# Kernel tuning notes

Measured on AMD Instinct MI355X. Metric: run time of the kernel, lower is better.

The kernel has to match this reference:

```python
import jax, jax.numpy as jnp
import numpy as np

NUM_SAMPLED = 8192
NUM_CLASSES = 50000
DIM = 512
BATCH = 8192


def _log_uniform_expected(ids, num_sampled, num_classes):
    # log-uniform sampler probability: P(c) = (log(c+2) - log(c+1)) / log(V+1)
    c = ids.astype(jnp.float32)
    p = (jnp.log(c + 2.0) - jnp.log(c + 1.0)) / jnp.log(float(num_classes + 1))
    # expected count under unique sampling of num_sampled candidates (as in TF)
    return -jnp.expm1(float(num_sampled) * jnp.log1p(-p))


def setup_inputs() -> dict:
    key = jax.random.key(0)
    k1, k2, k3, k4, k5 = jax.random.split(key, 5)
    inputs = jax.random.normal(k1, (BATCH, DIM), jnp.float32)
    labels = jax.random.randint(k2, (BATCH, 1), 0, NUM_CLASSES)
    kernel = jax.random.uniform(k3, (NUM_CLASSES, DIM), jnp.float32, -0.05, 0.05)
    bias = jax.random.uniform(k4, (NUM_CLASSES,), jnp.float32, -0.05, 0.05)
    sampled = jax.random.randint(k5, (NUM_SAMPLED,), 0, NUM_CLASSES)
    return {"inputs": inputs, "labels": labels, "kernel": kernel,
            "bias": bias, "sampled": sampled}


def reference(inputs, labels, kernel, bias, sampled):
    # tf.nn.sampled_softmax_loss (train branch), num_true=1,
    # log-uniform sampler, remove_accidental_hits=True.
    labels_flat = labels[:, 0]

    # true logits: gather one weight row per example, dot with input
    w_true = kernel[labels_flat]                      # [B, D]
    b_true = bias[labels_flat]                        # [B]
    true_logits = jnp.einsum('bd,bd->b', inputs, w_true) + b_true
    true_logits = true_logits - jnp.log(
        _log_uniform_expected(labels_flat, NUM_SAMPLED, NUM_CLASSES))

    # sampled logits: gather S candidate rows, small matmul [B,D]x[D,S]
    w_samp = kernel[sampled]                          # [S, D]
    b_samp = bias[sampled]                            # [S]
    sampled_logits = jnp.einsum('bd,sd->bs', inputs, w_samp) + b_samp[None, :]
    sampled_logits = sampled_logits - jnp.log(
        _log_uniform_expected(sampled, NUM_SAMPLED, NUM_CLASSES))

    # remove accidental hits: mask sampled candidates that equal the true label
    hits = labels_flat[:, None] == sampled[None, :]   # [B, S]
    sampled_logits = jnp.where(hits, -1e9, sampled_logits)

    # softmax CE with the true class at column 0
    logits = jnp.concatenate([true_logits[:, None], sampled_logits], axis=1)
    loss = jax.nn.logsumexp(logits, axis=1) - logits[:, 0]  # [B]
    return loss
```

## Files before the change

### kernel.cpp

```cpp
#include <hip/hip_runtime.h>
#include <hip/hip_bf16.h>
#include <cstdint>
#include <cstddef>

#define BATCH   8192
#define NSAMP   8192
#define DIM     512
#define NCLASS  50000

typedef __attribute__((ext_vector_type(8))) short bf16x8;
typedef __attribute__((ext_vector_type(4))) float f32x4;

__device__ __forceinline__ float neg_log_expected(int c) {
    double p = log1p(1.0 / (double)(c + 1)) / log((double)(NCLASS + 1));
    double e = -expm1((double)NSAMP * log1p(-p));
    return (float)(-log(e));
}

__device__ __forceinline__ unsigned short f2bf(float f) {
    __hip_bfloat16 h = __float2bfloat16(f);
    return *reinterpret_cast<unsigned short*>(&h);
}

__device__ __forceinline__ void gload_lds16(const void* g, void* l) {
    __builtin_amdgcn_global_load_lds(
        (const __attribute__((address_space(1))) void*)g,
        (__attribute__((address_space(3))) void*)l, 16, 0, 0);
}

__global__ void k_fused(const float* __restrict__ inputs, const int* __restrict__ labels,
                        const float* __restrict__ W, const float* __restrict__ bias,
                        __hip_bfloat16* __restrict__ Abf,
                        float* __restrict__ true_logit, float* __restrict__ row_sum) {
    int row = blockIdx.x;
    int t   = threadIdx.x;
    float4 v = reinterpret_cast<const float4*>(inputs + (size_t)row * DIM)[t];
    ushort4 u;
    u.x = f2bf(v.x); u.y = f2bf(v.y); u.z = f2bf(v.z); u.w = f2bf(v.w);
    reinterpret_cast<ushort4*>(Abf + (size_t)row * DIM)[t] = u;

    int lbl = labels[row];
    float4 w = reinterpret_cast<const float4*>(W + (size_t)lbl * DIM)[t];
    float dot = v.x * w.x + v.y * w.y + v.z * w.z + v.w * w.w;
    #pragma unroll
    for (int off = 32; off; off >>= 1) dot += __shfl_down(dot, off, 64);
    __shared__ float red[2];
    if ((t & 63) == 0) red[t >> 6] = dot;
    __syncthreads();
    if (t == 0) {
        float tl = red[0] + red[1] + bias[lbl] + neg_log_expected(lbl);
        true_logit[row] = tl;
        row_sum[row]    = __expf(tl);
    }
}

__global__ void k_gather(const float* __restrict__ W, const float* __restrict__ bias,
                         const int* __restrict__ sampled,
                         __hip_bfloat16* __restrict__ Bbf, float* __restrict__ adj) {
    int s   = blockIdx.x;
    int idx = sampled[s];
    float4 v = reinterpret_cast<const float4*>(W + (size_t)idx * DIM)[threadIdx.x];
    ushort4 u;
    u.x = f2bf(v.x); u.y = f2bf(v.y); u.z = f2bf(v.z); u.w = f2bf(v.w);
    reinterpret_cast<ushort4*>(Bbf + (size_t)s * DIM)[threadIdx.x] = u;
    if (threadIdx.x == 0) adj[s] = bias[idx] + neg_log_expected(idx);
}

__global__ __launch_bounds__(256, 4) void k_gemm(
    const __hip_bfloat16* __restrict__ A, const __hip_bfloat16* __restrict__ B,
    const float* __restrict__ adj, const int* __restrict__ labels,
    const int* __restrict__ sampled, float* __restrict__ row_sum) {
    __shared__ alignas(16) __hip_bfloat16 Asm[2][128 * 32];
    __shared__ alignas(16) __hip_bfloat16 Bsm[2][128 * 32];
    __shared__ float tsum[2][128];

    const int tid  = threadIdx.x;
    const int wave = tid >> 6;
    const int lane = tid & 63;
    const int wr   = wave >> 1;
    const int wc   = wave & 1;

    const int bid  = blockIdx.x;
    const int xcd  = bid & 7;
    const int u    = bid >> 3;
    const int rb   = xcd * 8 + (u & 7);
    const int cgrp = u >> 3;
    const int brow = rb * 128;

    const int srow = lane >> 2;
    const int sg   = (lane & 3) ^ ((lane >> 3) & 3);
    const int rsel = lane & 15;
    const int koff = ((lane >> 4) ^ ((lane >> 1) & 3)) * 8;

    f32x4 acc[4][4];
    #pragma unroll
    for (int m = 0; m < 4; ++m)
        #pragma unroll
        for (int n = 0; n < 4; ++n)
            acc[m][n] = (f32x4){0.f, 0.f, 0.f, 0.f};

    auto stage = [&](int g) {
        const int buf = g & 1, t = g >> 4, kt = g & 15;
        const int bcol = (cgrp * 4 + t) * 128;
        #pragma unroll
        for (int i = 0; i < 2; ++i) {
            const __hip_bfloat16* gA =
                A + (size_t)(brow + wave * 32 + i * 16 + srow) * DIM + kt * 32 + sg * 8;
            gload_lds16(gA, &Asm[buf][(wave * 32 + i * 16) * 32]);
            const __hip_bfloat16* gB =
                B + (size_t)(bcol + wave * 32 + i * 16 + srow) * DIM + kt * 32 + sg * 8;
            gload_lds16(gB, &Bsm[buf][(wave * 32 + i * 16) * 32]);
        }
    };

    auto body = [&](int buf) {
        bf16x8 a[4], b[4];
        #pragma unroll
        for (int m = 0; m < 4; ++m)
            a[m] = *reinterpret_cast<const bf16x8*>(
                &Asm[buf][(wr * 64 + m * 16 + rsel) * 32 + koff]);
        #pragma unroll
        for (int n = 0; n < 4; ++n)
            b[n] = *reinterpret_cast<const bf16x8*>(
                &Bsm[buf][(wc * 64 + n * 16 + rsel) * 32 + koff]);
        #pragma unroll
        for (int m = 0; m < 4; ++m)
            #pragma unroll
            for (int n = 0; n < 4; ++n)
                acc[m][n] = __builtin_amdgcn_mfma_f32_16x16x32_bf16(a[m], b[n], acc[m][n], 0, 0, 0);
    };

    auto epi = [&](int t) {
        const int bcol = (cgrp * 4 + t) * 128;
        int sv[4]; float aadj[4];
        #pragma unroll
        for (int n = 0; n < 4; ++n) {
            int col = bcol + wc * 64 + n * 16 + rsel;
            aadj[n] = adj[col];
            sv[n]   = sampled[col];
        }
        #pragma unroll
        for (int m = 0; m < 4; ++m) {
            #pragma unroll
            for (int r = 0; r < 4; ++r) {
                int lr  = wr * 64 + m * 16 + (lane >> 4) * 4 + r;
                int lbl = labels[brow + lr];
                float part = 0.f;
                #pragma unroll
                for (int n = 0; n < 4; ++n) {
                    float logit = acc[m][n][r] + aadj[n];
                    part += (sv[n] == lbl) ? 0.f : __expf(logit);
                }
                part += __shfl_xor(part, 1, 16);
                part += __shfl_xor(part, 2, 16);
                part += __shfl_xor(part, 4, 16);
                part += __shfl_xor(part, 8, 16);
                if (rsel == 0) tsum[wc][lr] = part;
            }
        }
        __syncthreads();
        if (tid < 128)
            atomicAdd(&row_sum[brow + tid], tsum[0][tid] + tsum[1][tid]);
        #pragma unroll
        for (int m = 0; m < 4; ++m)
            #pragma unroll
            for (int n = 0; n < 4; ++n)
                acc[m][n] = (f32x4){0.f, 0.f, 0.f, 0.f};
    };

    stage(0);
    __syncthreads();

    #pragma unroll 1
    for (int g = 0; g < 64; ++g) {
        if (g + 1 < 64) stage(g + 1);
        body(g & 1);
        if ((g & 15) == 15) epi(g >> 4);
        __syncthreads();
    }
}

__global__ void k_final(const float* __restrict__ row_sum,
                        const float* __restrict__ true_logit,
                        float* __restrict__ loss) {
    int i = blockIdx.x * blockDim.x + threadIdx.x;
    loss[i] = logf(row_sum[i]) - true_logit[i];
}

extern "C" void kernel_launch(void* const* d_in, const int* in_sizes, int n_in,
                              void* d_out, int out_size, void* d_ws, size_t ws_size,
                              hipStream_t stream) {
    const float* inputs  = (const float*)d_in[0];
    const int*   labels  = (const int*)d_in[1];
    const float* W       = (const float*)d_in[2];
    const float* bias    = (const float*)d_in[3];
    const int*   sampled = (const int*)d_in[4];
    float*       loss    = (float*)d_out;

    char* ws = (char*)d_ws;
    __hip_bfloat16* Abf = (__hip_bfloat16*)ws;
    __hip_bfloat16* Bbf = (__hip_bfloat16*)(ws + (size_t)BATCH * DIM * 2);
    float* adj        = (float*)(ws + (size_t)(BATCH + NSAMP) * DIM * 2);
    float* true_logit = adj + NSAMP;
    float* row_sum    = true_logit + BATCH;

    hipLaunchKernelGGL(k_fused, dim3(BATCH), dim3(128), 0, stream,
                       inputs, labels, W, bias, Abf, true_logit, row_sum);
    hipLaunchKernelGGL(k_gather, dim3(NSAMP), dim3(128), 0, stream,
                       W, bias, sampled, Bbf, adj);
    hipLaunchKernelGGL(k_gemm, dim3(1024), dim3(256), 0, stream,
                       Abf, Bbf, adj, labels, sampled, row_sum);
    hipLaunchKernelGGL(k_final, dim3(BATCH / 256), dim3(256), 0, stream,
                       row_sum, true_logit, loss);
}
```

Baseline: 125.0 us.

## Use 8 waves per GEMM block with smaller per-wave tiles and pointer-increment staging

Measured after the change: 136.8 us. +9.5%, slower.

```diff
diff --git a/kernel.cpp b/kernel.cpp
--- a/kernel.cpp
+++ b/kernel.cpp
@@ -66,7 +66,7 @@
     if (threadIdx.x == 0) adj[s] = bias[idx] + neg_log_expected(idx);
 }
 
-__global__ __launch_bounds__(256, 4) void k_gemm(
+__global__ __launch_bounds__(512, 6) void k_gemm(
     const __hip_bfloat16* __restrict__ A, const __hip_bfloat16* __restrict__ B,
     const float* __restrict__ adj, const int* __restrict__ labels,
     const int* __restrict__ sampled, float* __restrict__ row_sum) {
@@ -77,8 +77,8 @@
     const int tid  = threadIdx.x;
     const int wave = tid >> 6;
     const int lane = tid & 63;
-    const int wr   = wave >> 1;
-    const int wc   = wave & 1;
+    const int wm   = wave >> 1;
+    const int wn   = wave & 1;
 
     const int bid  = blockIdx.x;
     const int xcd  = bid & 7;
@@ -92,39 +92,39 @@
     const int rsel = lane & 15;
     const int koff = ((lane >> 4) ^ ((lane >> 1) & 3)) * 8;
 
-    f32x4 acc[4][4];
+    f32x4 acc[2][4];
     #pragma unroll
-    for (int m = 0; m < 4; ++m)
+    for (int m = 0; m < 2; ++m)
         #pragma unroll
         for (int n = 0; n < 4; ++n)
             acc[m][n] = (f32x4){0.f, 0.f, 0.f, 0.f};
 
-    auto stage = [&](int g) {
-        const int buf = g & 1, t = g >> 4, kt = g & 15;
-        const int bcol = (cgrp * 4 + t) * 128;
-        #pragma unroll
-        for (int i = 0; i < 2; ++i) {
-            const __hip_bfloat16* gA =
-                A + (size_t)(brow + wave * 32 + i * 16 + srow) * DIM + kt * 32 + sg * 8;
-            gload_lds16(gA, &Asm[buf][(wave * 32 + i * 16) * 32]);
-            const __hip_bfloat16* gB =
-                B + (size_t)(bcol + wave * 32 + i * 16 + srow) * DIM + kt * 32 + sg * 8;
-            gload_lds16(gB, &Bsm[buf][(wave * 32 + i * 16) * 32]);
-        }
+    const __hip_bfloat16* pa = A + (size_t)(brow + wave * 16 + srow) * DIM + sg * 8;
+    const __hip_bfloat16* pb = B + (size_t)(cgrp * 512 + wave * 16 + srow) * DIM + sg * 8;
+
+    auto stage = [&](int buf) {
+        gload_lds16(pa, &Asm[buf][(wave * 16) * 32]);
+        gload_lds16(pb, &Bsm[buf][(wave * 16) * 32]);
+    };
+    auto advance = [&](int snext) {
+        const bool tb = (snext & 15) == 0;
+        const ptrdiff_t dA = tb ? (ptrdiff_t)-480 : (ptrdiff_t)32;
+        const ptrdiff_t dB = tb ? (ptrdiff_t)(128 * DIM - 480) : (ptrdiff_t)32;
+        pa += dA; pb += dB;
     };
 
     auto body = [&](int buf) {
-        bf16x8 a[4], b[4];
-        #pragma unroll
-        for (int m = 0; m < 4; ++m)
+        bf16x8 a[2], b[4];
+        #pragma unroll
+        for (int m = 0; m < 2; ++m)
             a[m] = *reinterpret_cast<const bf16x8*>(
-                &Asm[buf][(wr * 64 + m * 16 + rsel) * 32 + koff]);
+                &Asm[buf][(wm * 32 + m * 16 + rsel) * 32 + koff]);
         #pragma unroll
         for (int n = 0; n < 4; ++n)
             b[n] = *reinterpret_cast<const bf16x8*>(
-                &Bsm[buf][(wc * 64 + n * 16 + rsel) * 32 + koff]);
-        #pragma unroll
-        for (int m = 0; m < 4; ++m)
+                &Bsm[buf][(wn * 64 + n * 16 + rsel) * 32 + koff]);
+        #pragma unroll
+        for (int m = 0; m < 2; ++m)
             #pragma unroll
             for (int n = 0; n < 4; ++n)
                 acc[m][n] = __builtin_amdgcn_mfma_f32_16x16x32_bf16(a[m], b[n], acc[m][n], 0, 0, 0);
@@ -135,15 +135,15 @@
         int sv[4]; float aadj[4];
         #pragma unroll
         for (int n = 0; n < 4; ++n) {
-            int col = bcol + wc * 64 + n * 16 + rsel;
+            int col = bcol + wn * 64 + n * 16 + rsel;
             aadj[n] = adj[col];
             sv[n]   = sampled[col];
         }
         #pragma unroll
-        for (int m = 0; m < 4; ++m) {
+        for (int m = 0; m < 2; ++m) {
             #pragma unroll
             for (int r = 0; r < 4; ++r) {
-                int lr  = wr * 64 + m * 16 + (lane >> 4) * 4 + r;
+                int lr  = wm * 32 + m * 16 + (lane >> 4) * 4 + r;
                 int lbl = labels[brow + lr];
                 float part = 0.f;
                 #pragma unroll
@@ -155,25 +155,26 @@
                 part += __shfl_xor(part, 2, 16);
                 part += __shfl_xor(part, 4, 16);
                 part += __shfl_xor(part, 8, 16);
-                if (rsel == 0) tsum[wc][lr] = part;
+                if (rsel == 0) tsum[wn][lr] = part;
             }
         }
         __syncthreads();
         if (tid < 128)
             atomicAdd(&row_sum[brow + tid], tsum[0][tid] + tsum[1][tid]);
         #pragma unroll
-        for (int m = 0; m < 4; ++m)
+        for (int m = 0; m < 2; ++m)
             #pragma unroll
             for (int n = 0; n < 4; ++n)
                 acc[m][n] = (f32x4){0.f, 0.f, 0.f, 0.f};
     };
 
     stage(0);
+    advance(1);
     __syncthreads();
 
     #pragma unroll 1
     for (int g = 0; g < 64; ++g) {
-        if (g + 1 < 64) stage(g + 1);
+        if (g < 63) { stage((g + 1) & 1); advance(g + 2); }
         body(g & 1);
         if ((g & 15) == 15) epi(g >> 4);
         __syncthreads();
@@ -208,7 +209,7 @@
                        inputs, labels, W, bias, Abf, true_logit, row_sum);
     hipLaunchKernelGGL(k_gather, dim3(NSAMP), dim3(128), 0, stream,
                        W, bias, sampled, Bbf, adj);
-    hipLaunchKernelGGL(k_gemm, dim3(1024), dim3(256), 0, stream,
+    hipLaunchKernelGGL(k_gemm, dim3(1024), dim3(512), 0, stream,
                        Abf, Bbf, adj, labels, sampled, row_sum);
     hipLaunchKernelGGL(k_final, dim3(BATCH / 256), dim3(256), 0, stream,
                        row_sum, true_logit, loss);
```

## Deduplicate sampled candidates via histogram and compact GEMM columns

Applied to the files above, without the earlier changes.

After: 125.9 us. No clear change (+0.8%).

```diff
diff --git a/kernel.cpp b/kernel.cpp
--- a/kernel.cpp
+++ b/kernel.cpp
@@ -7,6 +7,7 @@
 #define NSAMP   8192
 #define DIM     512
 #define NCLASS  50000
+#define HBINS   50176
 
 typedef __attribute__((ext_vector_type(8))) short bf16x8;
 typedef __attribute__((ext_vector_type(4))) float f32x4;
@@ -28,48 +29,120 @@
         (__attribute__((address_space(3))) void*)l, 16, 0, 0);
 }
 
-__global__ void k_fused(const float* __restrict__ inputs, const int* __restrict__ labels,
-                        const float* __restrict__ W, const float* __restrict__ bias,
-                        __hip_bfloat16* __restrict__ Abf,
-                        float* __restrict__ true_logit, float* __restrict__ row_sum) {
-    int row = blockIdx.x;
+__global__ void k_zero(int* __restrict__ hist) {
+    hist[blockIdx.x * 1024 + threadIdx.x] = 0;
+}
+__global__ void k_hist(const int* __restrict__ sampled, int* __restrict__ hist) {
+    atomicAdd(&hist[sampled[blockIdx.x * 1024 + threadIdx.x]], 1);
+}
+__global__ void k_scan1(const int* __restrict__ hist, int* __restrict__ btot) {
+    int b = blockIdx.x, t = threadIdx.x;
+    int c = b * 196 + t;
+    int x = (t < 196 && c < NCLASS && hist[c] > 0) ? 1 : 0;
+    int lane = t & 63, wv = t >> 6;
+    #pragma unroll
+    for (int off = 32; off; off >>= 1) x += __shfl_down(x, off, 64);
+    __shared__ int ws[4];
+    if (lane == 0) ws[wv] = x;
+    __syncthreads();
+    if (t == 0) btot[b] = ws[0] + ws[1] + ws[2] + ws[3];
+}
+__global__ void k_scan2(const int* __restrict__ btot, int* __restrict__ boff,
+                        int* __restrict__ meta) {
+    int t = threadIdx.x;
+    int v = btot[t];
+    int lane = t & 63, wv = t >> 6;
+    int x = v;
+    #pragma unroll
+    for (int off = 1; off < 64; off <<= 1) {
+        int y = __shfl_up(x, off, 64);
+        if (lane >= off) x += y;
+    }
+    __shared__ int ws[4];
+    if (lane == 63) ws[wv] = x;
+    __syncthreads();
+    int base = 0;
+    for (int w = 0; w < wv; ++w) base += ws[w];
+    boff[t] = base + x - v;
+    if (t == 255) {
+        int D = base + x;
+        meta[0] = D;
+        meta[1] = (D + 127) & ~127;
+    }
+}
+__global__ void k_scatter(const int* __restrict__ hist, const int* __restrict__ boff,
+                          int* __restrict__ didx) {
+    int b = blockIdx.x, t = threadIdx.x;
+    int c = b * 196 + t;
+    int ind = (t < 196 && c < NCLASS && hist[c] > 0) ? 1 : 0;
+    int lane = t & 63, wv = t >> 6;
+    int x = ind;
+    #pragma unroll
+    for (int off = 1; off < 64; off <<= 1) {
+        int y = __shfl_up(x, off, 64);
+        if (lane >= off) x += y;
+    }
+    __shared__ int ws[4];
+    if (lane == 63) ws[wv] = x;
+    __syncthreads();
+    int base = boff[b];
+    for (int w = 0; w < wv; ++w) base += ws[w];
+    if (ind) didx[base + x - 1] = c;
+}
+
+__global__ void k_prep(const float* __restrict__ inputs, const int* __restrict__ labels,
+                       const float* __restrict__ W, const float* __restrict__ bias,
+                       const int* __restrict__ hist, const int* __restrict__ didx,
+                       const int* __restrict__ meta,
+                       __hip_bfloat16* __restrict__ Abf, __hip_bfloat16* __restrict__ Bbf,
+                       float* __restrict__ adj,
+                       float* __restrict__ true_logit, float* __restrict__ row_sum) {
+    int bid = blockIdx.x;
     int t   = threadIdx.x;
-    float4 v = reinterpret_cast<const float4*>(inputs + (size_t)row * DIM)[t];
-    ushort4 u;
-    u.x = f2bf(v.x); u.y = f2bf(v.y); u.z = f2bf(v.z); u.w = f2bf(v.w);
-    reinterpret_cast<ushort4*>(Abf + (size_t)row * DIM)[t] = u;
-
-    int lbl = labels[row];
-    float4 w = reinterpret_cast<const float4*>(W + (size_t)lbl * DIM)[t];
-    float dot = v.x * w.x + v.y * w.y + v.z * w.z + v.w * w.w;
-    #pragma unroll
-    for (int off = 32; off; off >>= 1) dot += __shfl_down(dot, off, 64);
-    __shared__ float red[2];
-    if ((t & 63) == 0) red[t >> 6] = dot;
-    __syncthreads();
-    if (t == 0) {
-        float tl = red[0] + red[1] + bias[lbl] + neg_log_expected(lbl);
-        true_logit[row] = tl;
-        row_sum[row]    = __expf(tl);
-    }
-}
-
-__global__ void k_gather(const float* __restrict__ W, const float* __restrict__ bias,
-                         const int* __restrict__ sampled,
-                         __hip_bfloat16* __restrict__ Bbf, float* __restrict__ adj) {
-    int s   = blockIdx.x;
-    int idx = sampled[s];
-    float4 v = reinterpret_cast<const float4*>(W + (size_t)idx * DIM)[threadIdx.x];
-    ushort4 u;
-    u.x = f2bf(v.x); u.y = f2bf(v.y); u.z = f2bf(v.z); u.w = f2bf(v.w);
-    reinterpret_cast<ushort4*>(Bbf + (size_t)s * DIM)[threadIdx.x] = u;
-    if (threadIdx.x == 0) adj[s] = bias[idx] + neg_log_expected(idx);
+    if (bid < BATCH) {
+        int row = bid;
+        float4 v = reinterpret_cast<const float4*>(inputs + (size_t)row * DIM)[t];
+        ushort4 u;
+        u.x = f2bf(v.x); u.y = f2bf(v.y); u.z = f2bf(v.z); u.w = f2bf(v.w);
+        reinterpret_cast<ushort4*>(Abf + (size_t)row * DIM)[t] = u;
+
+        int lbl = labels[row];
+        float4 w = reinterpret_cast<const float4*>(W + (size_t)lbl * DIM)[t];
+        float dot = v.x * w.x + v.y * w.y + v.z * w.z + v.w * w.w;
+        #pragma unroll
+        for (int off = 32; off; off >>= 1) dot += __shfl_down(dot, off, 64);
+        __shared__ float red[2];
+        if ((t & 63) == 0) red[t >> 6] = dot;
+        __syncthreads();
+        if (t == 0) {
+            float tl = red[0] + red[1] + bias[lbl] + neg_log_expected(lbl);
+            true_logit[row] = tl;
+            row_sum[row]    = (1.0f - (float)hist[lbl]) * __expf(tl);
+        }
+    } else {
+        int s = bid - BATCH;
+        int D = meta[0], padD = meta[1];
+        if (s >= padD) return;
+        if (s < D) {
+            int idx = didx[s];
+            float4 v = reinterpret_cast<const float4*>(W + (size_t)idx * DIM)[t];
+            ushort4 u;
+            u.x = f2bf(v.x); u.y = f2bf(v.y); u.z = f2bf(v.z); u.w = f2bf(v.w);
+            reinterpret_cast<ushort4*>(Bbf + (size_t)s * DIM)[t] = u;
+            if (t == 0)
+                adj[s] = bias[idx] + neg_log_expected(idx) + logf((float)hist[idx]);
+        } else {
+            ushort4 z; z.x = z.y = z.z = z.w = 0;
+            reinterpret_cast<ushort4*>(Bbf + (size_t)s * DIM)[t] = z;
+            if (t == 0) adj[s] = -100000.0f;
+        }
+    }
 }
 
 __global__ __launch_bounds__(256, 4) void k_gemm(
     const __hip_bfloat16* __restrict__ A, const __hip_bfloat16* __restrict__ B,
     const float* __restrict__ adj, const int* __restrict__ labels,
-    const int* __restrict__ sampled, float* __restrict__ row_sum) {
+    const int* __restrict__ meta, float* __restrict__ row_sum) {
     __shared__ alignas(16) __hip_bfloat16 Asm[2][128 * 32];
     __shared__ alignas(16) __hip_bfloat16 Bsm[2][128 * 32];
     __shared__ float tsum[2][128];
@@ -87,6 +160,11 @@
     const int cgrp = u >> 3;
     const int brow = rb * 128;
 
+    const int nct = meta[1] >> 7;
+    const int ntl = (nct > cgrp) ? (((nct - cgrp - 1) >> 4) + 1) : 0;
+    if (ntl == 0) return;
+    const int nsteps = ntl << 4;
+
     const int srow = lane >> 2;
     const int sg   = (lane & 3) ^ ((lane >> 3) & 3);
     const int rsel = lane & 15;
@@ -101,7 +179,7 @@
 
     auto stage = [&](int g) {
         const int buf = g & 1, t = g >> 4, kt = g & 15;
-        const int bcol = (cgrp * 4 + t) * 128;
+        const int bcol = (cgrp + t * 16) << 7;
         #pragma unroll
         for (int i = 0; i < 2; ++i) {
             const __hip_bfloat16* gA =
@@ -130,27 +208,20 @@
                 acc[m][n] = __builtin_amdgcn_mfma_f32_16x16x32_bf16(a[m], b[n], acc[m][n], 0, 0, 0);
     };
 
-    auto epi = [&](int t) {
-        const int bcol = (cgrp * 4 + t) * 128;
-        int sv[4]; float aadj[4];
-        #pragma unroll
-        for (int n = 0; n < 4; ++n) {
-            int col = bcol + wc * 64 + n * 16 + rsel;
-            aadj[n] = adj[col];
-            sv[n]   = sampled[col];
-        }
+    auto epi = [&](int i) {
+        const int bcol = (cgrp + i * 16) << 7;
+        float aadj[4];
+        #pragma unroll
+        for (int n = 0; n < 4; ++n) aadj[n] = adj[bcol + wc * 64 + n * 16 + rsel];
         #pragma unroll
         for (int m = 0; m < 4; ++m) {
             #pragma unroll
             for (int r = 0; r < 4; ++r) {
-                int lr  = wr * 64 + m * 16 + (lane >> 4) * 4 + r;
-                int lbl = labels[brow + lr];
+                int lr = wr * 64 + m * 16 + (lane >> 4) * 4 + r;
                 float part = 0.f;
                 #pragma unroll
-                for (int n = 0; n < 4; ++n) {
-                    float logit = acc[m][n][r] + aadj[n];
-                    part += (sv[n] == lbl) ? 0.f : __expf(logit);
-                }
+                for (int n = 0; n < 4; ++n)
+                    part += __expf(acc[m][n][r] + aadj[n]);
                 part += __shfl_xor(part, 1, 16);
                 part += __shfl_xor(part, 2, 16);
                 part += __shfl_xor(part, 4, 16);
@@ -172,8 +243,8 @@
     __syncthreads();
 
     #pragma unroll 1
-    for (int g = 0; g < 64; ++g) {
-        if (g + 1 < 64) stage(g + 1);
+    for (int g = 0; g < nsteps; ++g) {
+        if (g + 1 < nsteps) stage(g + 1);
         body(g & 1);
         if ((g & 15) == 15) epi(g >> 4);
         __syncthreads();
@@ -200,16 +271,26 @@
     char* ws = (char*)d_ws;
     __hip_bfloat16* Abf = (__hip_bfloat16*)ws;
     __hip_bfloat16* Bbf = (__hip_bfloat16*)(ws + (size_t)BATCH * DIM * 2);
-    float* adj        = (float*)(ws + (size_t)(BATCH + NSAMP) * DIM * 2);
-    float* true_logit = adj + NSAMP;
-    float* row_sum    = true_logit + BATCH;
-
-    hipLaunchKernelGGL(k_fused, dim3(BATCH), dim3(128), 0, stream,
-                       inputs, labels, W, bias, Abf, true_logit, row_sum);
-    hipLaunchKernelGGL(k_gather, dim3(NSAMP), dim3(128), 0, stream,
-                       W, bias, sampled, Bbf, adj);
-    hipLaunchKernelGGL(k_gemm, dim3(1024), dim3(256), 0, stream,
-                       Abf, Bbf, adj, labels, sampled, row_sum);
-    hipLaunchKernelGGL(k_final, dim3(BATCH / 256), dim3(256), 0, stream,
+    size_t off = (size_t)(BATCH + NSAMP) * DIM * 2;
+    float* adj        = (float*)(ws + off);            off += NSAMP * 4;
+    float* true_logit = (float*)(ws + off);            off += BATCH * 4;
+    float* row_sum    = (float*)(ws + off);            off += BATCH * 4;
+    int*   hist       = (int*)(ws + off);              off += HBINS * 4;
+    int*   btot       = (int*)(ws + off);              off += 256 * 4;
+    int*   boff       = (int*)(ws + off);              off += 256 * 4;
+    int*   meta       = (int*)(ws + off);              off += 16;
+    int*   didx       = (int*)(ws + off);              off += NSAMP * 4;
+
+    hipLaunchKernelGGL(k_zero,    dim3(HBINS / 1024), dim3(1024), 0, stream, hist);
+    hipLaunchKernelGGL(k_hist,    dim3(NSAMP / 1024), dim3(1024), 0, stream, sampled, hist);
+    hipLaunchKernelGGL(k_scan1,   dim3(256), dim3(256), 0, stream, hist, btot);
+    hipLaunchKernelGGL(k_scan2,   dim3(1),   dim3(256), 0, stream, btot, boff, meta);
+    hipLaunchKernelGGL(k_scatter, dim3(256), dim3(256), 0, stream, hist, boff, didx);
+    hipLaunchKernelGGL(k_prep,    dim3(BATCH + NSAMP), dim3(128), 0, stream,
+                       inputs, labels, W, bias, hist, didx, meta,
+                       Abf, Bbf, adj, true_logit, row_sum);
+    hipLaunchKernelGGL(k_gemm,    dim3(1024), dim3(256), 0, stream,
+                       Abf, Bbf, adj, labels, meta, row_sum);
+    hipLaunchKernelGGL(k_final,   dim3(BATCH / 256), dim3(256), 0, stream,
                        row_sum, true_logit, loss);
 }
```
